# Kernel optimization log

Measured on AMD Instinct MI355X. Metric: run time of the kernel, lower is better.

## Reference

```python
import jax, jax.numpy as jnp
import numpy as np
from jax import lax

NT, TL = 32, 64           # num_trajs, traj_length
H, W, C = 84, 84, 4       # Atari frame stack
SIZE = 256                # LSTM hidden size
NOUT = 18                 # num_outputs
FEAT = 6 * 6 * 32         # after four stride-2 SAME convs: 84->42->21->11->6
DN = ('NHWC', 'HWIO', 'NHWC')


def setup_inputs() -> dict:
    key = jax.random.key(0)
    ks = jax.random.split(key, 8)
    d = {}
    d['inputs'] = jax.random.normal(ks[0], (NT * TL, H, W, C), jnp.float32)
    cin = C
    for i in range(4):
        d[f'w{i+1}'] = jax.random.normal(ks[1 + i], (3, 3, cin, 32), jnp.float32) * 0.1
        d[f'b{i+1}'] = jnp.zeros((32,), jnp.float32)
        cin = 32
    d['lstm_w'] = jax.random.normal(ks[5], (FEAT + SIZE, 4 * SIZE), jnp.float32) * 0.05
    d['lstm_b'] = jnp.zeros((4 * SIZE,), jnp.float32)
    d['fc_w'] = jax.random.normal(ks[6], (SIZE, NOUT), jnp.float32) * 0.01
    d['fc_b'] = jnp.zeros((NOUT,), jnp.float32)
    d['c0'] = jnp.zeros((NT, SIZE), jnp.float32)
    d['h0'] = jnp.zeros((NT, SIZE), jnp.float32)
    return d


def reference(inputs, w1, b1, w2, b2, w3, b3, w4, b4,
              lstm_w, lstm_b, fc_w, fc_b, c0, h0):
    x = inputs
    for w, b in ((w1, b1), (w2, b2), (w3, b3), (w4, b4)):
        x = jax.nn.elu(lax.conv_general_dilated(
            x, w, window_strides=(2, 2), padding='SAME',
            dimension_numbers=DN) + b)
    # [NT*TL, 6, 6, 32] -> [TL, NT, FEAT] (time-major for scan)
    xs = x.reshape(NT, TL, FEAT).transpose(1, 0, 2)

    def step(carry, xt):
        c, h = carry
        gates = jnp.concatenate([xt, h], axis=-1) @ lstm_w + lstm_b
        i, j, f, o = jnp.split(gates, 4, axis=-1)
        # BasicLSTMCell with forget_bias = 1.0
        new_c = c * jax.nn.sigmoid(f + 1.0) + jax.nn.sigmoid(i) * jnp.tanh(j)
        new_h = jnp.tanh(new_c) * jax.nn.sigmoid(o)
        return (new_c, new_h), new_h

    _, outs = lax.scan(step, (c0, h0), xs)          # outs: [TL, NT, SIZE]
    feats = outs.transpose(1, 0, 2).reshape(-1, SIZE)  # batch-major flatten
    logits = feats @ fc_w + fc_b                    # [NT*TL, NOUT]
    return logits
```

## Files before the change

### kernel.cpp

```cpp
#include <hip/hip_runtime.h>
#include <math.h>

#define NTRAJ 32
#define TLEN  64
#define BATCH (NTRAJ*TLEN)

__device__ __forceinline__ float eluf(float x){ return x > 0.f ? x : expm1f(x); }
__device__ __forceinline__ float sigmf(float x){ return 1.f/(1.f+expf(-x)); }

__global__ __launch_bounds__(256) void conv1_kernel(
    const float* __restrict__ in,
    const float* __restrict__ w,
    const float* __restrict__ b,
    float* __restrict__ out)
{
    int pos = blockIdx.x*256 + threadIdx.x;
    int n   = pos / (42*42);
    int rem = pos % (42*42);
    int oy  = rem / 42, ox = rem % 42;
    float acc[32];
    #pragma unroll
    for(int o=0;o<32;o++) acc[o] = b[o];
    for(int ky=0; ky<3; ky++){
        int iy = 2*oy + ky;
        if(iy >= 84) continue;
        for(int kx=0; kx<3; kx++){
            int ix = 2*ox + kx;
            if(ix >= 84) continue;
            float4 v = *(const float4*)(in + (((n*84 + iy)*84) + ix)*4);
            const float* wq = w + (ky*3 + kx)*128;
            #pragma unroll
            for(int o=0;o<32;o++) acc[o] += v.x*wq[o];
            #pragma unroll
            for(int o=0;o<32;o++) acc[o] += v.y*wq[32+o];
            #pragma unroll
            for(int o=0;o<32;o++) acc[o] += v.z*wq[64+o];
            #pragma unroll
            for(int o=0;o<32;o++) acc[o] += v.w*wq[96+o];
        }
    }
    const int NPOS = BATCH*42*42;
    #pragma unroll
    for(int o=0;o<32;o++) out[o*NPOS + pos] = eluf(acc[o]);
}

template<int IH, int IW, int OH, int OW, int PB>
__global__ __launch_bounds__(256) void convN_kernel(
    const float* __restrict__ in,
    const float* __restrict__ w,
    const float* __restrict__ b,
    float* __restrict__ out)
{
    const int IPLANE = BATCH*IH*IW;
    const int OPLANE = BATCH*OH*OW;
    int pos = blockIdx.x*256 + threadIdx.x;
    if(pos >= OPLANE) return;
    int n   = pos / (OH*OW);
    int rem = pos % (OH*OW);
    int oy  = rem / OW, ox = rem % OW;
    float acc[32];
    #pragma unroll
    for(int o=0;o<32;o++) acc[o] = b[o];
    for(int ky=0; ky<3; ky++){
        int iy = 2*oy + ky - PB;
        if(iy < 0 || iy >= IH) continue;
        for(int kx=0; kx<3; kx++){
            int ix = 2*ox + kx - PB;
            if(ix < 0 || ix >= IW) continue;
            const float* ip = in + (n*IH + iy)*IW + ix;
            const float* wp = w + (ky*3 + kx)*1024;
            for(int ci=0; ci<32; ci+=4){
                float x0 = ip[(ci+0)*IPLANE];
                float x1 = ip[(ci+1)*IPLANE];
                float x2 = ip[(ci+2)*IPLANE];
                float x3 = ip[(ci+3)*IPLANE];
                const float* wq = wp + ci*32;
                #pragma unroll
                for(int o=0;o<32;o++) acc[o] += x0*wq[o];
                #pragma unroll
                for(int o=0;o<32;o++) acc[o] += x1*wq[32+o];
                #pragma unroll
                for(int o=0;o<32;o++) acc[o] += x2*wq[64+o];
                #pragma unroll
                for(int o=0;o<32;o++) acc[o] += x3*wq[96+o];
            }
        }
    }
    #pragma unroll
    for(int o=0;o<32;o++) out[o*OPLANE + pos] = eluf(acc[o]);
}

__global__ __launch_bounds__(256) void relayout_kernel(
    const float* __restrict__ p4,
    float* __restrict__ at)
{
    int i = blockIdx.x*256 + threadIdx.x;
    int f = i >> 11, r = i & 2047;
    int s = f >> 5,  c = f & 31;
    int t = r >> 5,  n = r & 31;
    int nt = n*64 + t;
    at[i] = p4[c*(BATCH*36) + nt*36 + s];
}

__global__ __launch_bounds__(256) void gx_gemm_kernel(
    const float* __restrict__ at,
    const float* __restrict__ lw,
    const float* __restrict__ lb,
    float* __restrict__ gx)
{
    int lane = threadIdx.x & 63;
    int wv   = threadIdx.x >> 6;
    int r0   = blockIdx.x * 16;
    int oc   = blockIdx.y*256 + wv*64 + lane;
    float acc[16];
    float bias = lb[oc];
    #pragma unroll
    for(int i=0;i<16;i++) acc[i] = bias;
    #pragma unroll 4
    for(int k=0;k<1152;k++){
        float wval = lw[k*1024 + oc];
        const float* ap = at + k*2048 + r0;
        #pragma unroll
        for(int i=0;i<16;i++) acc[i] += ap[i] * wval;
    }
    #pragma unroll
    for(int i=0;i<16;i++) gx[(r0+i)*1024 + oc] = acc[i];
}

__global__ __launch_bounds__(256) void lstm_kernel(
    const float* __restrict__ gx,
    const float* __restrict__ lw,
    const float* __restrict__ c0,
    const float* __restrict__ h0,
    float* __restrict__ feats)
{
    __shared__ float hA[256], hB[256], gb[2][1024];
    const float* wh = lw + 1152*1024;
    int t  = threadIdx.x;
    int nA = blockIdx.x*2, nB = nA + 1;
    hA[t] = h0[nA*256 + t];
    hB[t] = h0[nB*256 + t];
    float cA = c0[nA*256 + t];
    float cB = c0[nB*256 + t];
    __syncthreads();
    for(int st=0; st<64; st++){
        float aA0=0.f,aA1=0.f,aA2=0.f,aA3=0.f;
        float aB0=0.f,aB1=0.f,aB2=0.f,aB3=0.f;
        #pragma unroll 4
        for(int k4=0;k4<64;k4++){
            float4 ha = *(const float4*)&hA[k4*4];
            float4 hb = *(const float4*)&hB[k4*4];
            const float* wp = wh + (k4*4)*1024 + 4*t;
            {   float4 w4 = *(const float4*)(wp);
                aA0 += ha.x*w4.x; aA1 += ha.x*w4.y; aA2 += ha.x*w4.z; aA3 += ha.x*w4.w;
                aB0 += hb.x*w4.x; aB1 += hb.x*w4.y; aB2 += hb.x*w4.z; aB3 += hb.x*w4.w; }
            {   float4 w4 = *(const float4*)(wp + 1024);
                aA0 += ha.y*w4.x; aA1 += ha.y*w4.y; aA2 += ha.y*w4.z; aA3 += ha.y*w4.w;
                aB0 += hb.y*w4.x; aB1 += hb.y*w4.y; aB2 += hb.y*w4.z; aB3 += hb.y*w4.w; }
            {   float4 w4 = *(const float4*)(wp + 2048);
                aA0 += ha.z*w4.x; aA1 += ha.z*w4.y; aA2 += ha.z*w4.z; aA3 += ha.z*w4.w;
                aB0 += hb.z*w4.x; aB1 += hb.z*w4.y; aB2 += hb.z*w4.z; aB3 += hb.z*w4.w; }
            {   float4 w4 = *(const float4*)(wp + 3072);
                aA0 += ha.w*w4.x; aA1 += ha.w*w4.y; aA2 += ha.w*w4.z; aA3 += ha.w*w4.w;
                aB0 += hb.w*w4.x; aB1 += hb.w*w4.y; aB2 += hb.w*w4.z; aB3 += hb.w*w4.w; }
        }
        float4 gA = *(const float4*)(gx + (st*32 + nA)*1024 + 4*t);
        float4 gB = *(const float4*)(gx + (st*32 + nB)*1024 + 4*t);
        gb[0][4*t+0] = aA0 + gA.x; gb[0][4*t+1] = aA1 + gA.y;
        gb[0][4*t+2] = aA2 + gA.z; gb[0][4*t+3] = aA3 + gA.w;
        gb[1][4*t+0] = aB0 + gB.x; gb[1][4*t+1] = aB1 + gB.y;
        gb[1][4*t+2] = aB2 + gB.z; gb[1][4*t+3] = aB3 + gB.w;
        __syncthreads();
        {
            float i_ = gb[0][t], j_ = gb[0][t+256], f_ = gb[0][t+512], o_ = gb[0][t+768];
            cA = cA*sigmf(f_+1.f) + sigmf(i_)*tanhf(j_);
            float h = tanhf(cA)*sigmf(o_);
            hA[t] = h;
            feats[(nA*64 + st)*256 + t] = h;
        }
        {
            float i_ = gb[1][t], j_ = gb[1][t+256], f_ = gb[1][t+512], o_ = gb[1][t+768];
            cB = cB*sigmf(f_+1.f) + sigmf(i_)*tanhf(j_);
            float h = tanhf(cB)*sigmf(o_);
            hB[t] = h;
            feats[(nB*64 + st)*256 + t] = h;
        }
        __syncthreads();
    }
}

__global__ __launch_bounds__(64) void fc_kernel(
    const float* __restrict__ feats, const float* __restrict__ fw,
    const float* __restrict__ fb,    float* __restrict__ out)
{
    __shared__ float h[256];
    int p = blockIdx.x, t = threadIdx.x;
    *(float4*)&h[t*4] = *(const float4*)(feats + p*256 + t*4);
    __syncthreads();
    if(t < 18){
        float acc = fb[t];
        for(int k=0;k<256;k++) acc += h[k]*fw[k*18 + t];
        out[p*18 + t] = acc;
    }
}

extern "C" void kernel_launch(void* const* d_in, const int* in_sizes, int n_in,
                              void* d_out, int out_size, void* d_ws, size_t ws_size,
                              hipStream_t stream) {
    const float* inp = (const float*)d_in[0];
    const float* w1  = (const float*)d_in[1];  const float* b1 = (const float*)d_in[2];
    const float* w2  = (const float*)d_in[3];  const float* b2 = (const float*)d_in[4];
    const float* w3  = (const float*)d_in[5];  const float* b3 = (const float*)d_in[6];
    const float* w4  = (const float*)d_in[7];  const float* b4 = (const float*)d_in[8];
    const float* lw  = (const float*)d_in[9];  const float* lb = (const float*)d_in[10];
    const float* fw  = (const float*)d_in[11]; const float* fb = (const float*)d_in[12];
    const float* c0  = (const float*)d_in[13]; const float* h0 = (const float*)d_in[14];
    float* out = (float*)d_out;
    float* ws  = (float*)d_ws;

    const size_t n1 = (size_t)32*3612672;
    const size_t n3 = (size_t)32*247808;
    const size_t n4 = (size_t)32*73728;

    float* p1 = ws;
    float* p2 = p1 + n1;
    float* p3 = ws;
    float* p4 = p3 + n3;
    float* at = p4 + n4;
    float* gxb   = at  + (size_t)1152*2048;
    float* feats = gxb + (size_t)2048*1024;

    conv1_kernel<<<14112,256,0,stream>>>(inp, w1, b1, p1);
    convN_kernel<42,42,21,21,0><<<3528,256,0,stream>>>(p1, w2, b2, p2);
    convN_kernel<21,21,11,11,1><<<968,256,0,stream>>>(p2, w3, b3, p3);
    convN_kernel<11,11, 6, 6,1><<<288,256,0,stream>>>(p3, w4, b4, p4);
    relayout_kernel<<<9216,256,0,stream>>>(p4, at);
    gx_gemm_kernel<<<dim3(128,4),256,0,stream>>>(at, lw, lb, gxb);
    lstm_kernel<<<16,256,0,stream>>>(gxb, lw, c0, h0, feats);
    fc_kernel<<<2048,64,0,stream>>>(feats, fw, fb, out);
}
```

Baseline: 2.049 ms.

## Split LSTM recurrence across 32 workgroups with LDS-resident weights and grid barrier

The LSTM recurrence is repartitioned so that each of 32 workgroups owns 8 hidden units (32 gate columns) for all trajectories. Each workgroup keeps its recurrent weight slice in LDS instead of streaming the full 1 MB recurrent matrix from global memory every step. Hidden state is exchanged through a double-buffered global buffer, and a spin-wait atomic grid barrier (reset inside the gx GEMM kernel) separates the steps. This adds per-step global synchronisation latency and relies on all 32 blocks being co-resident. The barrier has a bounded spin that breaks out after a fixed count, which could silently produce wrong results if it ever triggers.

```diff
diff --git a/kernel.cpp b/kernel.cpp
--- a/kernel.cpp
+++ b/kernel.cpp
@@ -106,8 +106,10 @@
     const float* __restrict__ at,
     const float* __restrict__ lw,
     const float* __restrict__ lb,
-    float* __restrict__ gx)
-{
+    float* __restrict__ gx,
+    unsigned int* __restrict__ bar)
+{
+    if(blockIdx.x == 0 && blockIdx.y == 0 && threadIdx.x == 0) *bar = 0u;
     int lane = threadIdx.x & 63;
     int wv   = threadIdx.x >> 6;
     int r0   = blockIdx.x * 16;
@@ -127,65 +129,97 @@
     for(int i=0;i<16;i++) gx[(r0+i)*1024 + oc] = acc[i];
 }
 
-__global__ __launch_bounds__(256) void lstm_kernel(
+__global__ __launch_bounds__(256) void lstm_coop_kernel(
     const float* __restrict__ gx,
     const float* __restrict__ lw,
     const float* __restrict__ c0,
     const float* __restrict__ h0,
-    float* __restrict__ feats)
-{
-    __shared__ float hA[256], hB[256], gb[2][1024];
+    float* __restrict__ feats,
+    float* __restrict__ hbuf,
+    unsigned int* __restrict__ bar)
+{
+    __shared__ float hs[32*256];
+    __shared__ float wl2[32*256];
+    float* const gl = hs;
+
+    const int wg = blockIdx.x;
+    const int t  = threadIdx.x;
+    const int c    = t & 31;
+    const int ngrp = t >> 3 >> 2;
+    const int gcol = (c>>3)*256 + wg*8 + (c&7);
     const float* wh = lw + 1152*1024;
-    int t  = threadIdx.x;
-    int nA = blockIdx.x*2, nB = nA + 1;
-    hA[t] = h0[nA*256 + t];
-    hB[t] = h0[nB*256 + t];
-    float cA = c0[nA*256 + t];
-    float cB = c0[nB*256 + t];
-    __syncthreads();
-    for(int st=0; st<64; st++){
-        float aA0=0.f,aA1=0.f,aA2=0.f,aA3=0.f;
-        float aB0=0.f,aB1=0.f,aB2=0.f,aB3=0.f;
+
+    #pragma unroll
+    for(int i=0;i<32;i++){
+        int e = t + 256*i;
+        int k = e >> 5, cc = e & 31;
+        int gc = (cc>>3)*256 + wg*8 + (cc&7);
+        wl2[(k>>1)*64 + cc*2 + (k&1)] = wh[k*1024 + gc];
+    }
+    const int un = t >> 3, uu = t & 7;
+    float cst = c0[un*256 + wg*8 + uu];
+
+    const float2* wv  = (const float2*)wl2;
+    float4* hs4 = (float4*)hs;
+
+    for(int st=0; st<64; ++st){
+        const float4* hp4 = (const float4*)((st == 0) ? h0 : (hbuf + ((st&1)^1)*8192));
+        #pragma unroll
+        for(int i=0;i<8;i++){
+            int q = t + 256*i;
+            hs4[q] = hp4[q];
+        }
+        int rbase = st*32 + ngrp*4;
+        float gx0 = gx[(rbase+0)*1024 + gcol];
+        float gx1 = gx[(rbase+1)*1024 + gcol];
+        float gx2 = gx[(rbase+2)*1024 + gcol];
+        float gx3 = gx[(rbase+3)*1024 + gcol];
+        __syncthreads();
+        float a0 = 0.f, a1 = 0.f, a2 = 0.f, a3 = 0.f;
+        const float4* h0r = hs4 + (ngrp*4+0)*64;
+        const float4* h1r = hs4 + (ngrp*4+1)*64;
+        const float4* h2r = hs4 + (ngrp*4+2)*64;
+        const float4* h3r = hs4 + (ngrp*4+3)*64;
         #pragma unroll 4
         for(int k4=0;k4<64;k4++){
-            float4 ha = *(const float4*)&hA[k4*4];
-            float4 hb = *(const float4*)&hB[k4*4];
-            const float* wp = wh + (k4*4)*1024 + 4*t;
-            {   float4 w4 = *(const float4*)(wp);
-                aA0 += ha.x*w4.x; aA1 += ha.x*w4.y; aA2 += ha.x*w4.z; aA3 += ha.x*w4.w;
-                aB0 += hb.x*w4.x; aB1 += hb.x*w4.y; aB2 += hb.x*w4.z; aB3 += hb.x*w4.w; }
-            {   float4 w4 = *(const float4*)(wp + 1024);
-                aA0 += ha.y*w4.x; aA1 += ha.y*w4.y; aA2 += ha.y*w4.z; aA3 += ha.y*w4.w;
-                aB0 += hb.y*w4.x; aB1 += hb.y*w4.y; aB2 += hb.y*w4.z; aB3 += hb.y*w4.w; }
-            {   float4 w4 = *(const float4*)(wp + 2048);
-                aA0 += ha.z*w4.x; aA1 += ha.z*w4.y; aA2 += ha.z*w4.z; aA3 += ha.z*w4.w;
-                aB0 += hb.z*w4.x; aB1 += hb.z*w4.y; aB2 += hb.z*w4.z; aB3 += hb.z*w4.w; }
-            {   float4 w4 = *(const float4*)(wp + 3072);
-                aA0 += ha.w*w4.x; aA1 += ha.w*w4.y; aA2 += ha.w*w4.z; aA3 += ha.w*w4.w;
-                aB0 += hb.w*w4.x; aB1 += hb.w*w4.y; aB2 += hb.w*w4.z; aB3 += hb.w*w4.w; }
-        }
-        float4 gA = *(const float4*)(gx + (st*32 + nA)*1024 + 4*t);
-        float4 gB = *(const float4*)(gx + (st*32 + nB)*1024 + 4*t);
-        gb[0][4*t+0] = aA0 + gA.x; gb[0][4*t+1] = aA1 + gA.y;
-        gb[0][4*t+2] = aA2 + gA.z; gb[0][4*t+3] = aA3 + gA.w;
-        gb[1][4*t+0] = aB0 + gB.x; gb[1][4*t+1] = aB1 + gB.y;
-        gb[1][4*t+2] = aB2 + gB.z; gb[1][4*t+3] = aB3 + gB.w;
+            float2 wa = wv[(2*k4+0)*32 + c];
+            float2 wb = wv[(2*k4+1)*32 + c];
+            float4 hv0 = h0r[k4], hv1 = h1r[k4], hv2 = h2r[k4], hv3 = h3r[k4];
+            a0 += hv0.x*wa.x + hv0.y*wa.y + hv0.z*wb.x + hv0.w*wb.y;
+            a1 += hv1.x*wa.x + hv1.y*wa.y + hv1.z*wb.x + hv1.w*wb.y;
+            a2 += hv2.x*wa.x + hv2.y*wa.y + hv2.z*wb.x + hv2.w*wb.y;
+            a3 += hv3.x*wa.x + hv3.y*wa.y + hv3.z*wb.x + hv3.w*wb.y;
+        }
+        __syncthreads();
+        gl[(ngrp*4+0)*33 + c] = a0 + gx0;
+        gl[(ngrp*4+1)*33 + c] = a1 + gx1;
+        gl[(ngrp*4+2)*33 + c] = a2 + gx2;
+        gl[(ngrp*4+3)*33 + c] = a3 + gx3;
         __syncthreads();
         {
-            float i_ = gb[0][t], j_ = gb[0][t+256], f_ = gb[0][t+512], o_ = gb[0][t+768];
-            cA = cA*sigmf(f_+1.f) + sigmf(i_)*tanhf(j_);
-            float h = tanhf(cA)*sigmf(o_);
-            hA[t] = h;
-            feats[(nA*64 + st)*256 + t] = h;
-        }
-        {
-            float i_ = gb[1][t], j_ = gb[1][t+256], f_ = gb[1][t+512], o_ = gb[1][t+768];
-            cB = cB*sigmf(f_+1.f) + sigmf(i_)*tanhf(j_);
-            float h = tanhf(cB)*sigmf(o_);
-            hB[t] = h;
-            feats[(nB*64 + st)*256 + t] = h;
-        }
-        __syncthreads();
+            float i_ = gl[un*33 +      uu];
+            float j_ = gl[un*33 +  8 + uu];
+            float f_ = gl[un*33 + 16 + uu];
+            float o_ = gl[un*33 + 24 + uu];
+            cst = cst*sigmf(f_ + 1.f) + sigmf(i_)*tanhf(j_);
+            float h = tanhf(cst)*sigmf(o_);
+            int col = wg*8 + uu;
+            hbuf[(st&1)*8192 + un*256 + col] = h;
+            feats[(un*64 + st)*256 + col]    = h;
+        }
+        if(st != 63){
+            __syncthreads();
+            if(t == 0){
+                unsigned tgt = (unsigned)(st+1)*32u;
+                __hip_atomic_fetch_add(bar, 1u, __ATOMIC_ACQ_REL, __HIP_MEMORY_SCOPE_AGENT);
+                unsigned spins = 0;
+                while(__hip_atomic_load(bar, __ATOMIC_ACQUIRE, __HIP_MEMORY_SCOPE_AGENT) < tgt){
+                    __builtin_amdgcn_s_sleep(2);
+                    if(++spins > 20000000u) break;
+                }
+            }
+            __syncthreads();
+        }
     }
 }
 
@@ -229,13 +263,15 @@
     float* at = p4 + n4;
     float* gxb   = at  + (size_t)1152*2048;
     float* feats = gxb + (size_t)2048*1024;
+    float* hbuf  = feats + (size_t)2048*256;
+    unsigned int* bar = (unsigned int*)(hbuf + 2*32*256);
 
     conv1_kernel<<<14112,256,0,stream>>>(inp, w1, b1, p1);
     convN_kernel<42,42,21,21,0><<<3528,256,0,stream>>>(p1, w2, b2, p2);
     convN_kernel<21,21,11,11,1><<<968,256,0,stream>>>(p2, w3, b3, p3);
     convN_kernel<11,11, 6, 6,1><<<288,256,0,stream>>>(p3, w4, b4, p4);
     relayout_kernel<<<9216,256,0,stream>>>(p4, at);
-    gx_gemm_kernel<<<dim3(128,4),256,0,stream>>>(at, lw, lb, gxb);
-    lstm_kernel<<<16,256,0,stream>>>(gxb, lw, c0, h0, feats);
+    gx_gemm_kernel<<<dim3(128,4),256,0,stream>>>(at, lw, lb, gxb, bar);
+    lstm_coop_kernel<<<32,256,0,stream>>>(gxb, lw, c0, h0, feats, hbuf, bar);
     fc_kernel<<<2048,64,0,stream>>>(feats, fw, fb, out);
 }
```

Measured after the change: 1.930 ms. -5.8%, faster.
